# Kernel tuning notes

Measured on AMD Instinct MI355X. Metric: run time of the kernel, lower is better.

The kernel has to match this reference:

```python
import jax, jax.numpy as jnp
import numpy as np

D = 768
SCALE = 1.0 / np.sqrt(D)  # 1/sqrt(question_size)
NEG_INF = -1e30


def setup_inputs() -> dict:
    key = jax.random.key(0)
    k1, k2, k3, k4 = jax.random.split(key, 4)
    B, Lc, Lq = 8, 2048, 1024
    context_hiddens = jax.random.normal(k1, (B, Lc, D), dtype=jnp.float32)
    context_mask = jnp.ones((B, Lc), dtype=jnp.float32)  # unused by forward (parity with original)
    question_hiddens = jax.random.normal(k2, (B, Lq, D), dtype=jnp.float32)
    question_mask = jax.random.randint(k3, (B, Lq), 0, 2, dtype=jnp.int32)
    # ensure at least one valid question token per row to avoid all -inf softmax
    question_mask = question_mask.at[:, 0].set(1)
    W = jax.random.normal(k4, (D, D), dtype=jnp.float32) * (1.0 / np.sqrt(D))
    b = jnp.zeros((D,), dtype=jnp.float32)
    return {
        "context_hiddens": context_hiddens,
        "context_mask": context_mask,
        "question_hiddens": question_hiddens,
        "question_mask": question_mask,
        "W": W,
        "b": b,
    }


def reference(context_hiddens, context_mask, question_hiddens, question_mask, W, b):
    # Linear projection of question hiddens: [B, Lq, D]
    query = jnp.einsum("bqd,ed->bqe", question_hiddens, W) + b
    # Bilinear scores: c_i' W q_j -> [B, Lc, Lq], scaled
    scores = jnp.einsum("bcd,bqd->bcq", context_hiddens, query) * SCALE
    # Masked softmax over question axis (mask==1 means valid)
    mask = question_mask[:, None, :].astype(jnp.bool_)  # [B, 1, Lq]
    scores = jnp.where(mask, scores, NEG_INF)
    attention_dist = jax.nn.softmax(scores, axis=2)
    # Weighted sum of question hiddens: [B, Lc, D]
    attn_output = jnp.einsum("bcq,bqd->bcd", attention_dist, question_hiddens)
    return jnp.concatenate([context_hiddens, attn_output], axis=2)  # [B, Lc, 2D]
```

## Files before the change

kernel.cpp:

```cpp
#include <hip/hip_runtime.h>
#include <hip/hip_bf16.h>
#include <cstdint>
#include <cstddef>

#define D 768
#define BATCH 8
#define LC 2048
#define LQ 1024
#define SCALE 0.03608439182435161f

typedef __attribute__((ext_vector_type(8))) short short8;
typedef __attribute__((ext_vector_type(4))) float floatx4;

__device__ __forceinline__ short f2bf(float f) {
    union { float f; uint32_t u; } v; v.f = f;
    uint32_t r = v.u + 0x7fffu + ((v.u >> 16) & 1u);
    return (short)(r >> 16);
}

__device__ __forceinline__ void gl_lds16(const short* g, short* l) {
    __builtin_amdgcn_global_load_lds(
        reinterpret_cast<const __attribute__((address_space(1))) unsigned int*>(
            reinterpret_cast<uintptr_t>(g)),
        reinterpret_cast<__attribute__((address_space(3))) unsigned int*>(
            reinterpret_cast<uintptr_t>(l)),
        16, 0, 0);
}

__device__ __forceinline__ void stage_tile(const short* gbase, int ld, int m0, int k0,
                                           short* lds, int tid) {
    const int r = tid >> 2, kc = (tid & 3) * 8;
    gl_lds16(gbase + (size_t)(m0 + r) * ld + k0 + kc, lds + tid * 8);
    gl_lds16(gbase + (size_t)(m0 + r + 64) * ld + k0 + kc, lds + 2048 + tid * 8);
}

__device__ __forceinline__ void mfma_tile_loop(
    const short* Ab, const short* Bb, int lda, int ldb, int K, int m0, int n0,
    short* sA, short* sB, int tid, floatx4 acc[4][4]) {
    const int w = tid >> 6, lane = tid & 63, l15 = lane & 15, quad = lane >> 4;
    const int wm = (w >> 1) * 64, wn = (w & 1) * 64;
    for (int k0 = 0; k0 < K; k0 += 32) {
        stage_tile(Ab, lda, m0, k0, sA, tid);
        stage_tile(Bb, ldb, n0, k0, sB, tid);
        __syncthreads();
        short8 af[4], bf[4];
#pragma unroll
        for (int mt = 0; mt < 4; ++mt)
            af[mt] = *reinterpret_cast<const short8*>(&sA[(wm + mt * 16 + l15) * 32 + quad * 8]);
#pragma unroll
        for (int nt = 0; nt < 4; ++nt)
            bf[nt] = *reinterpret_cast<const short8*>(&sB[(wn + nt * 16 + l15) * 32 + quad * 8]);
#pragma unroll
        for (int mt = 0; mt < 4; ++mt)
#pragma unroll
            for (int nt = 0; nt < 4; ++nt)
                acc[mt][nt] = __builtin_amdgcn_mfma_f32_16x16x32_bf16(af[mt], bf[nt], acc[mt][nt], 0, 0, 0);
        __syncthreads();
    }
}

__global__ void cast_w_kernel(const float* __restrict__ src, short* __restrict__ dst,
                              float* __restrict__ sums) {
    int i = blockIdx.x * 256 + threadIdx.x;
    if (i < 4096) {
        float4 z = {0.f, 0.f, 0.f, 0.f};
        reinterpret_cast<float4*>(sums)[i] = z;
    }
    float4 v = reinterpret_cast<const float4*>(src)[i];
    short4 o;
    o.x = f2bf(v.x); o.y = f2bf(v.y); o.z = f2bf(v.z); o.w = f2bf(v.w);
    reinterpret_cast<short4*>(dst)[i] = o;
}

__global__ void qh_pass_kernel(const float* __restrict__ qh, short* __restrict__ qh_b,
                               short* __restrict__ qhT) {
    __shared__ float tile[32][33];
    const int b = blockIdx.z;
    const int q0 = blockIdx.x * 32, d0 = blockIdx.y * 32;
    const int t = threadIdx.x;
    const int r = t >> 3, c = (t & 7) * 4;
    const float4 v = *reinterpret_cast<const float4*>(qh + ((size_t)b * LQ + q0 + r) * D + d0 + c);
    tile[r][c] = v.x; tile[r][c + 1] = v.y; tile[r][c + 2] = v.z; tile[r][c + 3] = v.w;
    short4 d;
    d.x = f2bf(v.x); d.y = f2bf(v.y); d.z = f2bf(v.z); d.w = f2bf(v.w);
    *reinterpret_cast<short4*>(qh_b + ((size_t)b * LQ + q0 + r) * D + d0 + c) = d;
    __syncthreads();
    short4 o;
    o.x = f2bf(tile[c][r]); o.y = f2bf(tile[c + 1][r]);
    o.z = f2bf(tile[c + 2][r]); o.w = f2bf(tile[c + 3][r]);
    *reinterpret_cast<short4*>(qhT + ((size_t)b * D + d0 + r) * LQ + q0 + c) = o;
}

__global__ __launch_bounds__(256, 2) void gemm1_kernel(
    const short* __restrict__ A, const short* __restrict__ W,
    const float* __restrict__ bias, short* __restrict__ Q) {
    __shared__ short sA[128 * 32];
    __shared__ short sB[128 * 32];
    const int m0 = blockIdx.x * 128, n0 = blockIdx.y * 128;
    const int tid = threadIdx.x;
    const int w = tid >> 6, lane = tid & 63, l15 = lane & 15, quad = lane >> 4;
    const int wm = (w >> 1) * 64, wn = (w & 1) * 64;
    floatx4 acc[4][4];
#pragma unroll
    for (int i = 0; i < 4; ++i)
#pragma unroll
        for (int j = 0; j < 4; ++j) { floatx4 z = {0.f, 0.f, 0.f, 0.f}; acc[i][j] = z; }
    mfma_tile_loop(A, W, D, D, D, m0, n0, sA, sB, tid, acc);
    float bv[4];
#pragma unroll
    for (int nt = 0; nt < 4; ++nt) bv[nt] = bias[n0 + wn + nt * 16 + l15];
#pragma unroll
    for (int mt = 0; mt < 4; ++mt)
#pragma unroll
        for (int r = 0; r < 4; ++r) {
            int row = m0 + wm + mt * 16 + quad * 4 + r;
#pragma unroll
            for (int nt = 0; nt < 4; ++nt)
                Q[(size_t)row * D + n0 + wn + nt * 16 + l15] = f2bf(acc[mt][nt][r] + bv[nt]);
        }
}

__global__ void ctx_pass_kernel(const float* __restrict__ ctx, float* __restrict__ out,
                                short* __restrict__ ctxb) {
    size_t i = (size_t)blockIdx.x * 256 + threadIdx.x;
    size_t row = i / 192;
    size_t c4 = i % 192;
    float4 v = reinterpret_cast<const float4*>(ctx)[i];
    reinterpret_cast<float4*>(out)[row * 384 + c4] = v;
    short4 o;
    o.x = f2bf(v.x); o.y = f2bf(v.y); o.z = f2bf(v.z); o.w = f2bf(v.w);
    reinterpret_cast<short4*>(ctxb)[i] = o;
}

__global__ __launch_bounds__(256, 2) void scores_gemm_kernel(
    const short* __restrict__ ctxb, const short* __restrict__ query_b,
    const int* __restrict__ qmask, short* __restrict__ P, float* __restrict__ sums) {
    __shared__ short sA[128 * 32];
    __shared__ short sB[128 * 32];
    const int b = blockIdx.z;
    const int m0 = blockIdx.x * 128, n0 = blockIdx.y * 128;
    const int tid = threadIdx.x;
    const int w = tid >> 6, lane = tid & 63, l15 = lane & 15, quad = lane >> 4;
    const int wm = (w >> 1) * 64, wn = (w & 1) * 64;
    floatx4 acc[4][4];
#pragma unroll
    for (int i = 0; i < 4; ++i)
#pragma unroll
        for (int j = 0; j < 4; ++j) { floatx4 z = {0.f, 0.f, 0.f, 0.f}; acc[i][j] = z; }
    mfma_tile_loop(ctxb + (size_t)b * LC * D, query_b + (size_t)b * LQ * D,
                   D, D, D, m0, n0, sA, sB, tid, acc);
    const int* mk = qmask + b * LQ;
    bool valid[4];
#pragma unroll
    for (int nt = 0; nt < 4; ++nt) valid[nt] = (mk[n0 + wn + nt * 16 + l15] != 0);
    short* Pb = P + (size_t)b * LC * LQ;
    float* sumb = sums + b * LC;
#pragma unroll
    for (int mt = 0; mt < 4; ++mt)
#pragma unroll
        for (int r = 0; r < 4; ++r) {
            size_t row = m0 + wm + mt * 16 + quad * 4 + r;
            float psum = 0.f;
#pragma unroll
            for (int nt = 0; nt < 4; ++nt) {
                float pv = valid[nt] ? __expf(acc[mt][nt][r] * SCALE) : 0.f;
                psum += pv;
                Pb[row * LQ + n0 + wn + nt * 16 + l15] = f2bf(pv);
            }
#pragma unroll
            for (int off = 1; off < 16; off <<= 1)
                psum += __shfl_xor(psum, off, 64);
            if (l15 == 0)
                atomicAdd(&sumb[row], psum);
        }
}

__global__ __launch_bounds__(256, 2) void gemm2_kernel(
    const short* __restrict__ P, const short* __restrict__ qhT,
    const float* __restrict__ sums, float* __restrict__ out) {
    __shared__ short sA[128 * 32];
    __shared__ short sB[128 * 32];
    const int b = blockIdx.z;
    const int m0 = blockIdx.x * 128, n0 = blockIdx.y * 128;
    const int tid = threadIdx.x;
    const int w = tid >> 6, lane = tid & 63, l15 = lane & 15, quad = lane >> 4;
    const int wm = (w >> 1) * 64, wn = (w & 1) * 64;
    floatx4 acc[4][4];
#pragma unroll
    for (int i = 0; i < 4; ++i)
#pragma unroll
        for (int j = 0; j < 4; ++j) { floatx4 z = {0.f, 0.f, 0.f, 0.f}; acc[i][j] = z; }
    mfma_tile_loop(P + (size_t)b * LC * LQ, qhT + (size_t)b * D * LQ,
                   LQ, LQ, LQ, m0, n0, sA, sB, tid, acc);
    const float* sumb = sums + b * LC;
#pragma unroll
    for (int mt = 0; mt < 4; ++mt)
#pragma unroll
        for (int r = 0; r < 4; ++r) {
            int lrow = m0 + wm + mt * 16 + quad * 4 + r;
            const float inv = 1.0f / sumb[lrow];
            size_t row = (size_t)b * LC + lrow;
#pragma unroll
            for (int nt = 0; nt < 4; ++nt)
                out[row * 1536 + 768 + n0 + wn + nt * 16 + l15] = acc[mt][nt][r] * inv;
        }
}

extern "C" void kernel_launch(void* const* d_in, const int* in_sizes, int n_in,
                              void* d_out, int out_size, void* d_ws, size_t ws_size,
                              hipStream_t stream) {
    const float* ctx = (const float*)d_in[0];
    const float* qh = (const float*)d_in[2];
    const int* qmask = (const int*)d_in[3];
    const float* Wf = (const float*)d_in[4];
    const float* bias = (const float*)d_in[5];
    float* out = (float*)d_out;

    char* ws = (char*)d_ws;
    short* W_b     = (short*)(ws);
    short* query_b = (short*)(ws + 1179648);
    short* qhT     = (short*)(ws + 13762560);
    short* ctx_b   = (short*)(ws + 26345472);
    short* P       = (short*)(ws + 51511296);
    float* sums    = (float*)(ws + 85065728);
    short* qh_b    = (short*)(ws + 51511296);

    cast_w_kernel<<<576, 256, 0, stream>>>(Wf, W_b, sums);
    qh_pass_kernel<<<dim3(32, 24, 8), 256, 0, stream>>>(qh, qh_b, qhT);
    ctx_pass_kernel<<<12288, 256, 0, stream>>>(ctx, out, ctx_b);
    gemm1_kernel<<<dim3(64, 6), 256, 0, stream>>>(qh_b, W_b, bias, query_b);
    scores_gemm_kernel<<<dim3(16, 8, 8), 256, 0, stream>>>(ctx_b, query_b, qmask, P, sums);
    gemm2_kernel<<<dim3(16, 6, 8), 256, 0, stream>>>(P, qhT, sums, out);
}
```

Before: 273.6 us.

## Use 256x256 triple-buffered direct-to-LDS GEMM loop for scores and PV GEMMs

Replaces the 128x128 synchronous tile loop in the scores and attention-output GEMMs with a 256x256 tile, 512-thread loop. The new loop triple-buffers K-slices loaded directly into LDS with XOR swizzling, interleaves the next tile's loads between MFMA halves, and raises wave priority around the MFMA bursts. Blocks are remapped so that batches are spread across XCDs. The intent is to hide global-load latency, remove LDS bank conflicts and raise arithmetic intensity. The cost is higher register and LDS pressure (96KB LDS, 128 accumulator floats per lane) and fewer blocks in the grid.

```diff
diff --git a/kernel.cpp b/kernel.cpp
--- a/kernel.cpp
+++ b/kernel.cpp
@@ -57,6 +57,86 @@
                 acc[mt][nt] = __builtin_amdgcn_mfma_f32_16x16x32_bf16(af[mt], bf[nt], acc[mt][nt], 0, 0, 0);
         __syncthreads();
     }
+}
+
+__device__ __forceinline__ void gemm256_loop(
+    const short* __restrict__ A, const short* __restrict__ B,
+    int lda, int ldb, int K, int m0, int n0,
+    short* lds, int tid, floatx4 acc[8][4]) {
+    const int lane = tid & 63, l15 = lane & 15, quad = lane >> 4;
+    const int w = tid >> 6, wm = w >> 2, wn = w & 3;
+
+    const int c0 = tid, c1 = tid + 512;
+    const int r0 = c0 >> 2, s0 = (c0 & 3) ^ (r0 & 3);
+    const int r1 = c1 >> 2, s1 = (c1 & 3) ^ (r1 & 3);
+    const short* gA0 = A + (size_t)(m0 + r0) * lda + s0 * 8;
+    const short* gA1 = A + (size_t)(m0 + r1) * lda + s1 * 8;
+    const short* gB0 = B + (size_t)(n0 + r0) * ldb + s0 * 8;
+    const short* gB1 = B + (size_t)(n0 + r1) * ldb + s1 * 8;
+    short* dA0 = lds + c0 * 8;
+    short* dA1 = lds + c1 * 8;
+    short* dB0 = lds + 8192 + c0 * 8;
+    short* dB1 = lds + 8192 + c1 * 8;
+
+    int aoff[8], boff[4];
+#pragma unroll
+    for (int mt = 0; mt < 8; ++mt) {
+        int r = wm * 128 + mt * 16 + l15;
+        aoff[mt] = r * 32 + ((quad ^ (r & 3)) * 8);
+    }
+#pragma unroll
+    for (int nt = 0; nt < 4; ++nt) {
+        int r = wn * 64 + nt * 16 + l15;
+        boff[nt] = 8192 + r * 32 + ((quad ^ (r & 3)) * 8);
+    }
+
+    const int NT = K >> 5;
+#define STAGE_A(t, bb) { gl_lds16(gA0 + (t) * 32, dA0 + (bb)); gl_lds16(gA1 + (t) * 32, dA1 + (bb)); }
+#define STAGE_B(t, bb) { gl_lds16(gB0 + (t) * 32, dB0 + (bb)); gl_lds16(gB1 + (t) * 32, dB1 + (bb)); }
+    STAGE_A(0, 0) STAGE_B(0, 0)
+    STAGE_A(1, 16384) STAGE_B(1, 16384)
+
+    for (int kt = 0; kt < NT; ++kt) {
+        const int cur = (kt % 3) * 16384;
+        const int nxt = ((kt + 2) % 3) * 16384;
+        if (kt + 1 < NT) { asm volatile("s_waitcnt vmcnt(4)" ::: "memory"); }
+        else             { asm volatile("s_waitcnt vmcnt(0)" ::: "memory"); }
+        __builtin_amdgcn_s_barrier();
+        __builtin_amdgcn_sched_barrier(0);
+
+        if (kt + 2 < NT) STAGE_A((kt + 2), nxt)
+
+        short8 af[8], bf[4];
+#pragma unroll
+        for (int mt = 0; mt < 8; ++mt)
+            af[mt] = *reinterpret_cast<const short8*>(lds + cur + aoff[mt]);
+#pragma unroll
+        for (int nt = 0; nt < 2; ++nt)
+            bf[nt] = *reinterpret_cast<const short8*>(lds + cur + boff[nt]);
+        __builtin_amdgcn_s_setprio(1);
+#pragma unroll
+        for (int mt = 0; mt < 8; ++mt)
+#pragma unroll
+            for (int nt = 0; nt < 2; ++nt)
+                acc[mt][nt] = __builtin_amdgcn_mfma_f32_16x16x32_bf16(af[mt], bf[nt], acc[mt][nt], 0, 0, 0);
+        __builtin_amdgcn_s_setprio(0);
+
+        if (kt + 2 < NT) STAGE_B((kt + 2), nxt)
+
+#pragma unroll
+        for (int nt = 2; nt < 4; ++nt)
+            bf[nt] = *reinterpret_cast<const short8*>(lds + cur + boff[nt]);
+        __builtin_amdgcn_s_setprio(1);
+#pragma unroll
+        for (int mt = 0; mt < 8; ++mt)
+#pragma unroll
+            for (int nt = 2; nt < 4; ++nt)
+                acc[mt][nt] = __builtin_amdgcn_mfma_f32_16x16x32_bf16(af[mt], bf[nt], acc[mt][nt], 0, 0, 0);
+        __builtin_amdgcn_s_setprio(0);
+        __builtin_amdgcn_sched_barrier(0);
+    }
+#undef STAGE_A
+#undef STAGE_B
 }
 
 __global__ void cast_w_kernel(const float* __restrict__ src, short* __restrict__ dst,
@@ -132,40 +212,43 @@
     reinterpret_cast<short4*>(ctxb)[i] = o;
 }
 
-__global__ __launch_bounds__(256, 2) void scores_gemm_kernel(
+__global__ __launch_bounds__(512, 2) void scores256_kernel(
     const short* __restrict__ ctxb, const short* __restrict__ query_b,
     const int* __restrict__ qmask, short* __restrict__ P, float* __restrict__ sums) {
-    __shared__ short sA[128 * 32];
-    __shared__ short sB[128 * 32];
-    const int b = blockIdx.z;
-    const int m0 = blockIdx.x * 128, n0 = blockIdx.y * 128;
+    __shared__ __align__(16) short lds[3 * 16384];
+    const int nb = ((blockIdx.x & 7) << 5) + (blockIdx.x >> 3);
+    const int b = nb >> 5, rem = nb & 31, by = rem >> 3, bx = rem & 7;
+    const int m0 = bx << 8, n0 = by << 8;
     const int tid = threadIdx.x;
-    const int w = tid >> 6, lane = tid & 63, l15 = lane & 15, quad = lane >> 4;
-    const int wm = (w >> 1) * 64, wn = (w & 1) * 64;
-    floatx4 acc[4][4];
-#pragma unroll
-    for (int i = 0; i < 4; ++i)
+    const int lane = tid & 63, l15 = lane & 15, quad = lane >> 4;
+    const int w = tid >> 6, wm = w >> 2, wn = w & 3;
+
+    floatx4 acc[8][4];
+#pragma unroll
+    for (int i = 0; i < 8; ++i)
 #pragma unroll
         for (int j = 0; j < 4; ++j) { floatx4 z = {0.f, 0.f, 0.f, 0.f}; acc[i][j] = z; }
-    mfma_tile_loop(ctxb + (size_t)b * LC * D, query_b + (size_t)b * LQ * D,
-                   D, D, D, m0, n0, sA, sB, tid, acc);
+
+    gemm256_loop(ctxb + (size_t)b * LC * D, query_b + (size_t)b * LQ * D,
+                 D, D, D, m0, n0, lds, tid, acc);
+
     const int* mk = qmask + b * LQ;
     bool valid[4];
 #pragma unroll
-    for (int nt = 0; nt < 4; ++nt) valid[nt] = (mk[n0 + wn + nt * 16 + l15] != 0);
+    for (int nt = 0; nt < 4; ++nt) valid[nt] = (mk[n0 + wn * 64 + nt * 16 + l15] != 0);
     short* Pb = P + (size_t)b * LC * LQ;
-    float* sumb = sums + b * LC;
-#pragma unroll
-    for (int mt = 0; mt < 4; ++mt)
-#pragma unroll
-        for (int r = 0; r < 4; ++r) {
-            size_t row = m0 + wm + mt * 16 + quad * 4 + r;
+    float* sumb = sums + (size_t)b * LC;
+#pragma unroll
+    for (int mt = 0; mt < 8; ++mt)
+#pragma unroll
+        for (int rr = 0; rr < 4; ++rr) {
+            int row = m0 + wm * 128 + mt * 16 + quad * 4 + rr;
             float psum = 0.f;
 #pragma unroll
             for (int nt = 0; nt < 4; ++nt) {
-                float pv = valid[nt] ? __expf(acc[mt][nt][r] * SCALE) : 0.f;
+                float pv = valid[nt] ? __expf(acc[mt][nt][rr] * SCALE) : 0.f;
                 psum += pv;
-                Pb[row * LQ + n0 + wn + nt * 16 + l15] = f2bf(pv);
+                Pb[(size_t)row * LQ + n0 + wn * 64 + nt * 16 + l15] = f2bf(pv);
             }
 #pragma unroll
             for (int off = 1; off < 16; off <<= 1)
@@ -175,34 +258,37 @@
         }
 }
 
-__global__ __launch_bounds__(256, 2) void gemm2_kernel(
+__global__ __launch_bounds__(512, 2) void gemm2_256_kernel(
     const short* __restrict__ P, const short* __restrict__ qhT,
     const float* __restrict__ sums, float* __restrict__ out) {
-    __shared__ short sA[128 * 32];
-    __shared__ short sB[128 * 32];
-    const int b = blockIdx.z;
-    const int m0 = blockIdx.x * 128, n0 = blockIdx.y * 128;
+    __shared__ __align__(16) short lds[3 * 16384];
+    const int nb = (blockIdx.x & 7) * 24 + (blockIdx.x >> 3);
+    const int b = nb / 24, rem = nb % 24, by = rem >> 3, bx = rem & 7;
+    const int m0 = bx << 8, n0 = by << 8;
     const int tid = threadIdx.x;
-    const int w = tid >> 6, lane = tid & 63, l15 = lane & 15, quad = lane >> 4;
-    const int wm = (w >> 1) * 64, wn = (w & 1) * 64;
-    floatx4 acc[4][4];
-#pragma unroll
-    for (int i = 0; i < 4; ++i)
+    const int lane = tid & 63, l15 = lane & 15, quad = lane >> 4;
+    const int w = tid >> 6, wm = w >> 2, wn = w & 3;
+
+    floatx4 acc[8][4];
+#pragma unroll
+    for (int i = 0; i < 8; ++i)
 #pragma unroll
         for (int j = 0; j < 4; ++j) { floatx4 z = {0.f, 0.f, 0.f, 0.f}; acc[i][j] = z; }
-    mfma_tile_loop(P + (size_t)b * LC * LQ, qhT + (size_t)b * D * LQ,
-                   LQ, LQ, LQ, m0, n0, sA, sB, tid, acc);
-    const float* sumb = sums + b * LC;
-#pragma unroll
-    for (int mt = 0; mt < 4; ++mt)
-#pragma unroll
-        for (int r = 0; r < 4; ++r) {
-            int lrow = m0 + wm + mt * 16 + quad * 4 + r;
+
+    gemm256_loop(P + (size_t)b * LC * LQ, qhT + (size_t)b * D * LQ,
+                 LQ, LQ, LQ, m0, n0, lds, tid, acc);
+
+    const float* sumb = sums + (size_t)b * LC;
+#pragma unroll
+    for (int mt = 0; mt < 8; ++mt)
+#pragma unroll
+        for (int rr = 0; rr < 4; ++rr) {
+            int lrow = m0 + wm * 128 + mt * 16 + quad * 4 + rr;
             const float inv = 1.0f / sumb[lrow];
-            size_t row = (size_t)b * LC + lrow;
+            size_t rowoff = ((size_t)b * LC + lrow) * 1536 + 768;
 #pragma unroll
             for (int nt = 0; nt < 4; ++nt)
-                out[row * 1536 + 768 + n0 + wn + nt * 16 + l15] = acc[mt][nt][r] * inv;
+                out[rowoff + n0 + wn * 64 + nt * 16 + l15] = acc[mt][nt][rr] * inv;
         }
 }
 
@@ -229,6 +315,6 @@
     qh_pass_kernel<<<dim3(32, 24, 8), 256, 0, stream>>>(qh, qh_b, qhT);
     ctx_pass_kernel<<<12288, 256, 0, stream>>>(ctx, out, ctx_b);
     gemm1_kernel<<<dim3(64, 6), 256, 0, stream>>>(qh_b, W_b, bias, query_b);
-    scores_gemm_kernel<<<dim3(16, 8, 8), 256, 0, stream>>>(ctx_b, query_b, qmask, P, sums);
-    gemm2_kernel<<<dim3(16, 6, 8), 256, 0, stream>>>(P, qhT, sums, out);
-}
+    scores256_kernel<<<dim3(256), dim3(512), 0, stream>>>(ctx_b, query_b, qmask, P, sums);
+    gemm2_256_kernel<<<dim3(192), dim3(512), 0, stream>>>(P, qhT, sums, out);
+}
```

After: 265.8 us. 1.03x faster.
